# Kernel tuning notes

Measured on AMD Instinct MI355X. Metric: run time of the kernel, lower is better.

Reference implementation:

```python
import jax, jax.numpy as jnp
import numpy as np

SOFTMAX_SCALE = 10.0  # self.softmax_scale
EPS = 1e-4


def _patches(img, k=3):
    # img: [H, W, C] -> patches laid out as conv filters [k, k, C, L], L = H*W
    # (matches tf.image.extract_patches SAME/stride1 + reshape + transpose([0,2,3,4,1]))
    H, W, C = img.shape
    pad = (k - 1) // 2
    xp = jnp.pad(img, ((pad, pad), (pad, pad), (0, 0)))
    pat = jnp.stack([jnp.stack([xp[p:p + H, q:q + W] for q in range(k)]) for p in range(k)])
    # pat: [k, k, H, W, C] -> [k, k, C, H*W]; L index is row-major (h*W + w) like TF reshape
    return pat.transpose(0, 1, 4, 2, 3).reshape(k, k, C, H * W)


def _normed(p):
    # per-patch L2 normalization over the k*k*C axes (axes 0,1,2)
    return p / jnp.maximum(jnp.sqrt(jnp.sum(p * p, axis=(0, 1, 2))), EPS)


def _corr_recon(a, b, k=3):
    # a, b: [H', W', C] shifted feature maps
    Hp, Wp, C = a.shape
    L = Hp * Wp
    pa = _patches(a, k)  # [k,k,C,L]
    pb = _patches(b, k)
    y = (_normed(pa) * _normed(pb)).reshape(k * k * C, L)
    att = y.T @ y                                   # [L, L] patch-correlation scores
    att = jax.nn.softmax(att.reshape(1, Hp, Wp, L) * SOFTMAX_SCALE, axis=3)
    dn = ('NHWC', 'HWIO', 'NHWC')
    # tf.nn.conv2d_transpose(att, filters=[k,k,C,L], stride=1, SAME); rate=1 so /rate**2 is a no-op
    ya = jax.lax.conv_transpose(att, pa, (1, 1), 'SAME', dimension_numbers=dn, transpose_kernel=True)[0]
    yb = jax.lax.conv_transpose(att, pb, (1, 1), 'SAME', dimension_numbers=dn, transpose_kernel=True)[0]
    return ya, yb  # each [H', W', C]


def _ecattn_single(xi):
    # xi: [H, W, C]
    left, right = xi[:-1], xi[1:]          # vertical neighbor pair, [H-1, W, C]
    top, bottom = xi[:, 1:], xi[:, :-1]    # horizontal neighbor pair, [H, W-1, C]
    yl, yr = _corr_recon(left, right)
    ylr = jnp.concatenate([yr[:1], (yr[1:] + yl[:-1]) * 0.5, yl[-1:]], axis=0)   # [H, W, C]
    yt, yb = _corr_recon(top, bottom)
    ytb = jnp.concatenate([yt[:, :1], (yt[:, 1:] + yb[:, :-1]) * 0.5, yb[:, -1:]], axis=1)  # [H, W, C]
    return (ylr + ytb) * 0.5


def setup_inputs() -> dict:
    key = jax.random.key(0)
    k1, k2 = jax.random.split(key)
    B, H, W, C = 4, 32, 32, 256
    x = jax.random.normal(k1, (B, H, W, C), dtype=jnp.float32)
    mask = jax.random.uniform(k2, (B, H, W, 1), dtype=jnp.float32)
    return {'x': x, 'mask': mask}


def reference(x, mask):
    # mask is accepted by the layer's call() but unused inside contextualAttention
    return jax.vmap(_ecattn_single)(x)
```

## Files before the change

### kernel.cpp

```cpp
#include <hip/hip_runtime.h>


typedef _Float16 half8 __attribute__((ext_vector_type(8)));
typedef _Float16 half8u __attribute__((ext_vector_type(8), aligned(4)));
typedef _Float16 half4h __attribute__((ext_vector_type(4)));
typedef _Float16 half4u __attribute__((ext_vector_type(4), aligned(8)));
typedef float floatx4 __attribute__((ext_vector_type(4)));

constexpr int NL = 992, NC = 256, NC2 = 512;
constexpr int NLL = NL * NL;
constexpr int OFF_ABT = 0;
constexpr int OFF_MH  = OFF_ABT + NL * NC2 / 2;
constexpr int OFF_SA  = OFF_MH + NL * NC / 2;
constexpr int OFF_SB  = OFF_SA + 1024;
constexpr int OFF_INV = OFF_SA + 2048;
constexpr int OFF_Y   = OFF_SA + 3072;
constexpr int OFF_B0  = OFF_Y + NL * NC2;
constexpr int OFF_B1  = OFF_B0 + NLL / 2;
constexpr int TSTRIDE = OFF_B1 + NLL / 2;

__device__ __forceinline__ void gload16(const void* g, void* l) {
    __builtin_amdgcn_global_load_lds(
        (const __attribute__((address_space(1))) unsigned int*)g,
        (__attribute__((address_space(3))) unsigned int*)(unsigned long)(uintptr_t)l,
        16, 0, 0);
}

__global__ __launch_bounds__(256) void k_stage(const float* __restrict__ x,
                                               float* __restrict__ ws) {
    const int t = blockIdx.x & 7;
    const int l0 = (blockIdx.x >> 3) * 32;
    const int s = t >> 1, o = t & 1;
    float* wst = ws + (size_t)t * TSTRIDE;
    _Float16* __restrict__ ABt = (_Float16*)(wst + OFF_ABT);
    _Float16* __restrict__ Mh = (_Float16*)(wst + OFF_MH);
    __shared__ float Ta[32 * 33], Tb[32 * 33];
    const int tid = threadIdx.x;
    const int li = tid >> 3, cq = tid & 7;
    const int l = l0 + li;
    int aoff, boff;
    if (o == 0) {
        const int lh = l >> 5, lw = l & 31;
        aoff = ((s * 32 + lh) * 32 + lw) * NC;
        boff = aoff + 32 * NC;
    } else {
        const int lh = l / 31, lw = l - lh * 31;
        boff = ((s * 32 + lh) * 32 + lw) * NC;
        aoff = boff + NC;
    }
    float sa = 0.0f, sb = 0.0f;
    for (int cc = 0; cc < 8; ++cc) {
        const int c0 = cc * 32;
        const float4 a4 = *(const float4*)&x[aoff + c0 + cq * 4];
        const float4 b4 = *(const float4*)&x[boff + c0 + cq * 4];
        half4h m;
        m[0] = (_Float16)(a4.x * b4.x); m[1] = (_Float16)(a4.y * b4.y);
        m[2] = (_Float16)(a4.z * b4.z); m[3] = (_Float16)(a4.w * b4.w);
        *(half4u*)&Mh[l * NC + c0 + cq * 4] = m;
        sa += a4.x * a4.x + a4.y * a4.y + a4.z * a4.z + a4.w * a4.w;
        sb += b4.x * b4.x + b4.y * b4.y + b4.z * b4.z + b4.w * b4.w;
        __syncthreads();
        Ta[(cq * 4 + 0) * 33 + li] = a4.x; Tb[(cq * 4 + 0) * 33 + li] = b4.x;
        Ta[(cq * 4 + 1) * 33 + li] = a4.y; Tb[(cq * 4 + 1) * 33 + li] = b4.y;
        Ta[(cq * 4 + 2) * 33 + li] = a4.z; Tb[(cq * 4 + 2) * 33 + li] = b4.z;
        Ta[(cq * 4 + 3) * 33 + li] = a4.w; Tb[(cq * 4 + 3) * 33 + li] = b4.w;
        __syncthreads();
        const int ci = li, lq = cq;
        half4h ha, hb;
#pragma unroll
        for (int j = 0; j < 4; ++j) {
            ha[j] = (_Float16)Ta[ci * 33 + lq * 4 + j];
            hb[j] = (_Float16)Tb[ci * 33 + lq * 4 + j];
        }
        *(half4u*)&ABt[(c0 + ci) * NL + l0 + lq * 4] = ha;
        *(half4u*)&ABt[(NC + c0 + ci) * NL + l0 + lq * 4] = hb;
    }
#pragma unroll
    for (int off = 4; off > 0; off >>= 1) {
        sa += __shfl_down(sa, off, 8);
        sb += __shfl_down(sb, off, 8);
    }
    if (cq == 0) {
        wst[OFF_SA + l] = sa;
        wst[OFF_SB + l] = sb;
    }
}

__global__ __launch_bounds__(1024) void k_inv(float* __restrict__ ws) {
    const int t = blockIdx.x;
    const int l = threadIdx.x;
    if (l >= NL) return;
    const int o = t & 1;
    const int Hp = o ? 32 : 31, Wp = o ? 31 : 32;
    float* wst = ws + (size_t)t * TSTRIDE;
    const int h = l / Wp, w = l - h * Wp;
    float na2 = 0.0f, nb2 = 0.0f;
#pragma unroll
    for (int dh = -1; dh <= 1; ++dh)
#pragma unroll
        for (int dw = -1; dw <= 1; ++dw) {
            const int hh = h + dh, ww = w + dw;
            if ((unsigned)hh < (unsigned)Hp && (unsigned)ww < (unsigned)Wp) {
                const int ll = hh * Wp + ww;
                na2 += wst[OFF_SA + ll];
                nb2 += wst[OFF_SB + ll];
            }
        }
    const float na = fmaxf(sqrtf(na2), 1e-4f);
    const float nb = fmaxf(sqrtf(nb2), 1e-4f);
    wst[OFF_INV + l] = 1.0f / (na * nb);
}

__global__ __launch_bounds__(256) void k_gram(float* __restrict__ ws) {
    const int t = blockIdx.x & 7;
    const int u = blockIdx.x >> 3;
    const int i0 = (u >> 3) * 128, j0 = (u & 7) * 128;
    float* wst = ws + (size_t)t * TSTRIDE;
    const _Float16* __restrict__ M = (const _Float16*)(wst + OFF_MH);
    _Float16* __restrict__ S = (_Float16*)(wst + OFF_B0);
    __shared__ __align__(16) _Float16 As[128 * 32];
    __shared__ __align__(16) _Float16 Bs[128 * 32];
    const int tid = threadIdx.x;
    const int wave = tid >> 6, lane = tid & 63;
    const int wm = wave & 1, wn = wave >> 1;
    const int l15 = lane & 15, quad = lane >> 4;
    floatx4 acc[4][4] = {};
    const int srow = tid >> 2;
    const int scol = (tid & 3) * 8;
    for (int k0 = 0; k0 < NC; k0 += 32) {
        __syncthreads();
        if (i0 + srow < NL)      gload16(&M[(i0 + srow) * NC + k0 + scol], &As[srow * 32 + scol]);
        if (i0 + 64 + srow < NL) gload16(&M[(i0 + 64 + srow) * NC + k0 + scol], &As[(64 + srow) * 32 + scol]);
        if (j0 + srow < NL)      gload16(&M[(j0 + srow) * NC + k0 + scol], &Bs[srow * 32 + scol]);
        if (j0 + 64 + srow < NL) gload16(&M[(j0 + 64 + srow) * NC + k0 + scol], &Bs[(64 + srow) * 32 + scol]);
        __syncthreads();
        half8 a[4], b[4];
#pragma unroll
        for (int mt = 0; mt < 4; ++mt) a[mt] = *(const half8*)&As[(wm * 64 + mt * 16 + l15) * 32 + quad * 8];
#pragma unroll
        for (int nt = 0; nt < 4; ++nt) b[nt] = *(const half8*)&Bs[(wn * 64 + nt * 16 + l15) * 32 + quad * 8];
#pragma unroll
        for (int mt = 0; mt < 4; ++mt)
#pragma unroll
            for (int nt = 0; nt < 4; ++nt)
                acc[mt][nt] = __builtin_amdgcn_mfma_f32_16x16x32_f16(a[mt], b[nt], acc[mt][nt], 0, 0, 0);
    }
#pragma unroll
    for (int mt = 0; mt < 4; ++mt)
#pragma unroll
        for (int nt = 0; nt < 4; ++nt)
#pragma unroll
            for (int r = 0; r < 4; ++r) {
                const int row = i0 + wm * 64 + mt * 16 + quad * 4 + r;
                const int col = j0 + wn * 64 + nt * 16 + l15;
                if (row < NL && col < NL) S[row * NL + col] = (_Float16)acc[mt][nt][r];
            }
}

template<int WP, int HP>
__device__ __forceinline__ void softmax9_body(float* __restrict__ wst,
                                              const int l1, const int tid) {
    const _Float16* __restrict__ S = (const _Float16*)(wst + OFF_B0);
    const float* __restrict__ inv = wst + OFF_INV;
    _Float16* __restrict__ Ph = (_Float16*)(wst + OFF_B1);
    const int c0 = tid * 4;
    const int h1 = l1 / WP, w1 = l1 % WP;
    float lg[4] = {-3.0e38f, -3.0e38f, -3.0e38f, -3.0e38f};
    float mx = -3.0e38f;
    if (tid < 248) {
        int hc[4], wc[4];
#pragma unroll
        for (int j = 0; j < 4; ++j) { hc[j] = (c0 + j) / WP; wc[j] = (c0 + j) % WP; }
        float g[4] = {0.f, 0.f, 0.f, 0.f};
        const _Float16* base = S + l1 * NL + c0;
#pragma unroll
        for (int dh = -1; dh <= 1; ++dh) {
            const bool oh1 = (unsigned)(h1 + dh) < (unsigned)HP;
#pragma unroll
            for (int dw = -1; dw <= 1; ++dw) {
                const int sh = dh * WP + dw;
                const int par = sh & 1;
                const bool ok1 = oh1 && (unsigned)(w1 + dw) < (unsigned)WP;
                const half8u v = *(const half8u*)(base + sh * (NL + 1) - par);
#pragma unroll
                for (int j = 0; j < 4; ++j) {
                    const bool ok = ok1 && (unsigned)(hc[j] + dh) < (unsigned)HP &&
                                           (unsigned)(wc[j] + dw) < (unsigned)WP;
                    if (ok) g[j] += (float)v[j + par];
                }
            }
        }
        const float inv1 = inv[l1] * 10.0f;
#pragma unroll
        for (int j = 0; j < 4; ++j) {
            lg[j] = g[j] * inv1 * inv[c0 + j];
            mx = fmaxf(mx, lg[j]);
        }
    }
    __shared__ float red[4];
    const int wave = tid >> 6, lane = tid & 63;
#pragma unroll
    for (int off = 32; off > 0; off >>= 1) mx = fmaxf(mx, __shfl_down(mx, off));
    if (lane == 0) red[wave] = mx;
    __syncthreads();
    mx = fmaxf(fmaxf(red[0], red[1]), fmaxf(red[2], red[3]));
    __syncthreads();
    float e[4];
    float sum = 0.0f;
#pragma unroll
    for (int j = 0; j < 4; ++j) { e[j] = __expf(lg[j] - mx); sum += e[j]; }
    if (tid >= 248) sum = 0.0f;
#pragma unroll
    for (int off = 32; off > 0; off >>= 1) sum += __shfl_down(sum, off);
    if (lane == 0) red[wave] = sum;
    __syncthreads();
    sum = red[0] + red[1] + red[2] + red[3];
    const float rs = 1.0f / sum;
    if (tid < 248) {
        half4h o;
#pragma unroll
        for (int j = 0; j < 4; ++j) o[j] = (_Float16)(e[j] * rs);
        *(half4u*)(Ph + l1 * NL + c0) = o;
    }
}

__global__ __launch_bounds__(256) void k_softmax9(float* __restrict__ ws) {
    const int t = blockIdx.x & 7;
    const int l1 = blockIdx.x >> 3;
    float* wst = ws + (size_t)t * TSTRIDE;
    if (t & 1) softmax9_body<31, 32>(wst, l1, threadIdx.x);
    else       softmax9_body<32, 31>(wst, l1, threadIdx.x);
}

template<int WP, int HP>
__device__ __forceinline__ void band9p_body(float* __restrict__ wst,
                                            const int m, const int tid) {
    if (tid >= 248) return;
    const _Float16* __restrict__ P = (const _Float16*)(wst + OFF_B1);
    _Float16* __restrict__ W = (_Float16*)(wst + OFF_B0);
    const int c0 = tid * 4;
    const int hm = m / WP, wm = m % WP;
    int hc[4], wc[4];
#pragma unroll
    for (int j = 0; j < 4; ++j) { hc[j] = (c0 + j) / WP; wc[j] = (c0 + j) % WP; }
    float acc[4] = {0.f, 0.f, 0.f, 0.f};
    const _Float16* base = P + m * NL + c0;
#pragma unroll
    for (int dh = -1; dh <= 1; ++dh) {
        const bool oh1 = (unsigned)(hm + dh) < (unsigned)HP;
#pragma unroll
        for (int dw = -1; dw <= 1; ++dw) {
            const int sh = dh * WP + dw;
            const int par = sh & 1;
            const bool ok1 = oh1 && (unsigned)(wm + dw) < (unsigned)WP;
            const half8u v = *(const half8u*)(base + sh * (NL + 1) - par);
#pragma unroll
            for (int j = 0; j < 4; ++j) {
                const bool ok = ok1 && (unsigned)(hc[j] + dh) < (unsigned)HP &&
                                       (unsigned)(wc[j] + dw) < (unsigned)WP;
                if (ok) acc[j] += (float)v[j + par];
            }
        }
    }
    half4h o;
#pragma unroll
    for (int j = 0; j < 4; ++j) o[j] = (_Float16)acc[j];
    *(half4u*)(W + m * NL + c0) = o;
}

__global__ __launch_bounds__(256) void k_band9p(float* __restrict__ ws) {
    const int t = blockIdx.x & 7;
    const int m = blockIdx.x >> 3;
    float* wst = ws + (size_t)t * TSTRIDE;
    if (t & 1) band9p_body<31, 32>(wst, m, threadIdx.x);
    else       band9p_body<32, 31>(wst, m, threadIdx.x);
}

__global__ __launch_bounds__(256) void k_recon(float* __restrict__ ws) {
    const int t = blockIdx.x & 7;
    const int u = blockIdx.x >> 3;
    const int i0 = (u >> 2) * 128, j0 = (u & 3) * 128;
    float* wst = ws + (size_t)t * TSTRIDE;
    const _Float16* __restrict__ Wm = (const _Float16*)(wst + OFF_B0);
    const _Float16* __restrict__ ABt = (const _Float16*)(wst + OFF_ABT);
    float* __restrict__ Y = wst + OFF_Y;
    __shared__ __align__(16) _Float16 As[128 * 32];
    __shared__ __align__(16) _Float16 Bs[128 * 32];
    const int tid = threadIdx.x;
    const int wave = tid >> 6, lane = tid & 63;
    const int wm = wave & 1, wn = wave >> 1;
    const int l15 = lane & 15, quad = lane >> 4;
    floatx4 acc[4][4] = {};
    const int srow = tid >> 2;
    const int scol = (tid & 3) * 8;
    for (int k0 = 0; k0 < NL; k0 += 32) {
        __syncthreads();
        if (i0 + srow < NL)      gload16(&Wm[(i0 + srow) * NL + k0 + scol], &As[srow * 32 + scol]);
        if (i0 + 64 + srow < NL) gload16(&Wm[(i0 + 64 + srow) * NL + k0 + scol], &As[(64 + srow) * 32 + scol]);
        gload16(&ABt[(j0 + srow) * NL + k0 + scol], &Bs[srow * 32 + scol]);
        gload16(&ABt[(j0 + 64 + srow) * NL + k0 + scol], &Bs[(64 + srow) * 32 + scol]);
        __syncthreads();
        half8 a[4], b[4];
#pragma unroll
        for (int mt = 0; mt < 4; ++mt) a[mt] = *(const half8*)&As[(wm * 64 + mt * 16 + l15) * 32 + quad * 8];
#pragma unroll
        for (int nt = 0; nt < 4; ++nt) b[nt] = *(const half8*)&Bs[(wn * 64 + nt * 16 + l15) * 32 + quad * 8];
#pragma unroll
        for (int mt = 0; mt < 4; ++mt)
#pragma unroll
            for (int nt = 0; nt < 4; ++nt)
                acc[mt][nt] = __builtin_amdgcn_mfma_f32_16x16x32_f16(a[mt], b[nt], acc[mt][nt], 0, 0, 0);
    }
#pragma unroll
    for (int mt = 0; mt < 4; ++mt)
#pragma unroll
        for (int nt = 0; nt < 4; ++nt)
#pragma unroll
            for (int r = 0; r < 4; ++r) {
                const int row = i0 + wm * 64 + mt * 16 + quad * 4 + r;
                const int col = j0 + wn * 64 + nt * 16 + l15;
                if (row < NL) Y[row * NC2 + col] = acc[mt][nt][r];
            }
}

__global__ __launch_bounds__(256) void k_combine(float* __restrict__ out,
                                                 const float* __restrict__ ws) {
    const int idx = blockIdx.x;
    const int s = idx >> 10;
    const int hw = idx & 1023;
    const int h = hw >> 5, w = hw & 31;
    const int c = threadIdx.x;
    const float* Ylr = ws + (size_t)(2 * s) * TSTRIDE + OFF_Y;
    const float* Ytb = ws + (size_t)(2 * s + 1) * TSTRIDE + OFF_Y;
    float v = 0.0f;
    if (h < 31) v += Ylr[(h * 32 + w) * NC2 + NC + c] * (h == 0 ? 1.0f : 0.5f);
    if (h >= 1) v += Ylr[((h - 1) * 32 + w) * NC2 + c] * (h == 31 ? 1.0f : 0.5f);
    if (w < 31) v += Ytb[(h * 31 + w) * NC2 + c] * (w == 0 ? 1.0f : 0.5f);
    if (w >= 1) v += Ytb[(h * 31 + (w - 1)) * NC2 + NC + c] * (w == 31 ? 1.0f : 0.5f);
    out[(size_t)idx * NC + c] = v * 0.5f;
}

extern "C" void kernel_launch(void* const* d_in, const int* in_sizes, int n_in,
                              void* d_out, int out_size, void* d_ws, size_t ws_size,
                              hipStream_t stream) {
    const float* x = (const float*)d_in[0];
    float* out = (float*)d_out;
    float* ws = (float*)d_ws;

    hipLaunchKernelGGL(k_stage,    dim3(8 * 31), dim3(256),  0, stream, x, ws);
    hipLaunchKernelGGL(k_inv,      dim3(8),      dim3(1024), 0, stream, ws);
    hipLaunchKernelGGL(k_gram,     dim3(8 * 64), dim3(256),  0, stream, ws);
    hipLaunchKernelGGL(k_softmax9, dim3(8 * NL), dim3(256),  0, stream, ws);
    hipLaunchKernelGGL(k_band9p,   dim3(8 * NL), dim3(256),  0, stream, ws);
    hipLaunchKernelGGL(k_recon,    dim3(8 * 32), dim3(256),  0, stream, ws);
    hipLaunchKernelGGL(k_combine,  dim3(4096),   dim3(256),  0, stream, out, ws);
}
```

Measured before the change: 149.4 us.

## Shrink gram/recon tiles to 64x64, fold norm kernel into gram, store Y in fp16

The Gram and reconstruction GEMMs move from 128x128 to 64x64 output tiles, giving four times as many blocks so more CUs are busy; the Gram kernel also switches to a K step of 64. The separate inverse-norm kernel is removed and its work is done by block u==0 of the Gram kernel, saving one launch. The reconstruction output Y is stored as fp16 instead of fp32, halving its workspace and the traffic read by the combine kernel, at some precision cost. Smaller tiles lower data reuse per block.

```diff
diff --git a/kernel.cpp b/kernel.cpp
--- a/kernel.cpp
+++ b/kernel.cpp
@@ -15,7 +15,7 @@
 constexpr int OFF_SB  = OFF_SA + 1024;
 constexpr int OFF_INV = OFF_SA + 2048;
 constexpr int OFF_Y   = OFF_SA + 3072;
-constexpr int OFF_B0  = OFF_Y + NL * NC2;
+constexpr int OFF_B0  = OFF_Y + NL * NC2 / 2;
 constexpr int OFF_B1  = OFF_B0 + NLL / 2;
 constexpr int TSTRIDE = OFF_B1 + NLL / 2;
 
@@ -86,73 +86,80 @@
     }
 }
 
-__global__ __launch_bounds__(1024) void k_inv(float* __restrict__ ws) {
-    const int t = blockIdx.x;
-    const int l = threadIdx.x;
-    if (l >= NL) return;
-    const int o = t & 1;
-    const int Hp = o ? 32 : 31, Wp = o ? 31 : 32;
-    float* wst = ws + (size_t)t * TSTRIDE;
-    const int h = l / Wp, w = l - h * Wp;
-    float na2 = 0.0f, nb2 = 0.0f;
-#pragma unroll
-    for (int dh = -1; dh <= 1; ++dh)
-#pragma unroll
-        for (int dw = -1; dw <= 1; ++dw) {
-            const int hh = h + dh, ww = w + dw;
-            if ((unsigned)hh < (unsigned)Hp && (unsigned)ww < (unsigned)Wp) {
-                const int ll = hh * Wp + ww;
-                na2 += wst[OFF_SA + ll];
-                nb2 += wst[OFF_SB + ll];
-            }
-        }
-    const float na = fmaxf(sqrtf(na2), 1e-4f);
-    const float nb = fmaxf(sqrtf(nb2), 1e-4f);
-    wst[OFF_INV + l] = 1.0f / (na * nb);
-}
-
 __global__ __launch_bounds__(256) void k_gram(float* __restrict__ ws) {
     const int t = blockIdx.x & 7;
     const int u = blockIdx.x >> 3;
-    const int i0 = (u >> 3) * 128, j0 = (u & 7) * 128;
+    const int i0 = (u >> 4) * 64, j0 = (u & 15) * 64;
     float* wst = ws + (size_t)t * TSTRIDE;
     const _Float16* __restrict__ M = (const _Float16*)(wst + OFF_MH);
     _Float16* __restrict__ S = (_Float16*)(wst + OFF_B0);
-    __shared__ __align__(16) _Float16 As[128 * 32];
-    __shared__ __align__(16) _Float16 Bs[128 * 32];
     const int tid = threadIdx.x;
+
+    if (u == 0) {
+        const int o = t & 1;
+        const int Hp = o ? 32 : 31, Wp = o ? 31 : 32;
+#pragma unroll
+        for (int q = 0; q < 4; ++q) {
+            const int l = tid + q * 256;
+            if (l < NL) {
+                const int h = l / Wp, w = l - h * Wp;
+                float na2 = 0.0f, nb2 = 0.0f;
+#pragma unroll
+                for (int dh = -1; dh <= 1; ++dh)
+#pragma unroll
+                    for (int dw = -1; dw <= 1; ++dw) {
+                        const int hh = h + dh, ww = w + dw;
+                        if ((unsigned)hh < (unsigned)Hp && (unsigned)ww < (unsigned)Wp) {
+                            const int ll = hh * Wp + ww;
+                            na2 += wst[OFF_SA + ll];
+                            nb2 += wst[OFF_SB + ll];
+                        }
+                    }
+                const float na = fmaxf(sqrtf(na2), 1e-4f);
+                const float nb = fmaxf(sqrtf(nb2), 1e-4f);
+                wst[OFF_INV + l] = 1.0f / (na * nb);
+            }
+        }
+    }
+
+    __shared__ __align__(16) _Float16 As[64 * 64];
+    __shared__ __align__(16) _Float16 Bs[64 * 64];
     const int wave = tid >> 6, lane = tid & 63;
     const int wm = wave & 1, wn = wave >> 1;
     const int l15 = lane & 15, quad = lane >> 4;
-    floatx4 acc[4][4] = {};
-    const int srow = tid >> 2;
-    const int scol = (tid & 3) * 8;
-    for (int k0 = 0; k0 < NC; k0 += 32) {
-        __syncthreads();
-        if (i0 + srow < NL)      gload16(&M[(i0 + srow) * NC + k0 + scol], &As[srow * 32 + scol]);
-        if (i0 + 64 + srow < NL) gload16(&M[(i0 + 64 + srow) * NC + k0 + scol], &As[(64 + srow) * 32 + scol]);
-        if (j0 + srow < NL)      gload16(&M[(j0 + srow) * NC + k0 + scol], &Bs[srow * 32 + scol]);
-        if (j0 + 64 + srow < NL) gload16(&M[(j0 + 64 + srow) * NC + k0 + scol], &Bs[(64 + srow) * 32 + scol]);
-        __syncthreads();
-        half8 a[4], b[4];
-#pragma unroll
-        for (int mt = 0; mt < 4; ++mt) a[mt] = *(const half8*)&As[(wm * 64 + mt * 16 + l15) * 32 + quad * 8];
-#pragma unroll
-        for (int nt = 0; nt < 4; ++nt) b[nt] = *(const half8*)&Bs[(wn * 64 + nt * 16 + l15) * 32 + quad * 8];
-#pragma unroll
-        for (int mt = 0; mt < 4; ++mt)
-#pragma unroll
-            for (int nt = 0; nt < 4; ++nt)
-                acc[mt][nt] = __builtin_amdgcn_mfma_f32_16x16x32_f16(a[mt], b[nt], acc[mt][nt], 0, 0, 0);
-    }
-#pragma unroll
-    for (int mt = 0; mt < 4; ++mt)
-#pragma unroll
-        for (int nt = 0; nt < 4; ++nt)
+    floatx4 acc[2][2] = {};
+    for (int k0 = 0; k0 < NC; k0 += 64) {
+        __syncthreads();
+#pragma unroll
+        for (int rr = 0; rr < 2; ++rr) {
+            const int slot = tid + rr * 256;
+            const int row = slot >> 3, cg = (slot & 7) * 8;
+            if (i0 + row < NL) gload16(&M[(i0 + row) * NC + k0 + cg], &As[row * 64 + cg]);
+            if (j0 + row < NL) gload16(&M[(j0 + row) * NC + k0 + cg], &Bs[row * 64 + cg]);
+        }
+        __syncthreads();
+#pragma unroll
+        for (int kk = 0; kk < 2; ++kk) {
+            half8 a[2], b[2];
+#pragma unroll
+            for (int mt = 0; mt < 2; ++mt) a[mt] = *(const half8*)&As[(wm * 32 + mt * 16 + l15) * 64 + kk * 32 + quad * 8];
+#pragma unroll
+            for (int nt = 0; nt < 2; ++nt) b[nt] = *(const half8*)&Bs[(wn * 32 + nt * 16 + l15) * 64 + kk * 32 + quad * 8];
+#pragma unroll
+            for (int mt = 0; mt < 2; ++mt)
+#pragma unroll
+                for (int nt = 0; nt < 2; ++nt)
+                    acc[mt][nt] = __builtin_amdgcn_mfma_f32_16x16x32_f16(a[mt], b[nt], acc[mt][nt], 0, 0, 0);
+        }
+    }
+#pragma unroll
+    for (int mt = 0; mt < 2; ++mt)
+#pragma unroll
+        for (int nt = 0; nt < 2; ++nt)
 #pragma unroll
             for (int r = 0; r < 4; ++r) {
-                const int row = i0 + wm * 64 + mt * 16 + quad * 4 + r;
-                const int col = j0 + wn * 64 + nt * 16 + l15;
+                const int row = i0 + wm * 32 + mt * 16 + quad * 4 + r;
+                const int col = j0 + wn * 32 + nt * 16 + l15;
                 if (row < NL && col < NL) S[row * NL + col] = (_Float16)acc[mt][nt][r];
             }
 }
@@ -279,47 +286,44 @@
 __global__ __launch_bounds__(256) void k_recon(float* __restrict__ ws) {
     const int t = blockIdx.x & 7;
     const int u = blockIdx.x >> 3;
-    const int i0 = (u >> 2) * 128, j0 = (u & 3) * 128;
+    const int i0 = (u >> 3) * 64, j0 = (u & 7) * 64;
     float* wst = ws + (size_t)t * TSTRIDE;
     const _Float16* __restrict__ Wm = (const _Float16*)(wst + OFF_B0);
     const _Float16* __restrict__ ABt = (const _Float16*)(wst + OFF_ABT);
-    float* __restrict__ Y = wst + OFF_Y;
-    __shared__ __align__(16) _Float16 As[128 * 32];
-    __shared__ __align__(16) _Float16 Bs[128 * 32];
+    _Float16* __restrict__ Y = (_Float16*)(wst + OFF_Y);
+    __shared__ __align__(16) _Float16 As[64 * 32];
+    __shared__ __align__(16) _Float16 Bs[64 * 32];
     const int tid = threadIdx.x;
     const int wave = tid >> 6, lane = tid & 63;
     const int wm = wave & 1, wn = wave >> 1;
     const int l15 = lane & 15, quad = lane >> 4;
-    floatx4 acc[4][4] = {};
-    const int srow = tid >> 2;
-    const int scol = (tid & 3) * 8;
+    floatx4 acc[2][2] = {};
+    const int row = tid >> 2, cg = (tid & 3) * 8;
     for (int k0 = 0; k0 < NL; k0 += 32) {
         __syncthreads();
-        if (i0 + srow < NL)      gload16(&Wm[(i0 + srow) * NL + k0 + scol], &As[srow * 32 + scol]);
-        if (i0 + 64 + srow < NL) gload16(&Wm[(i0 + 64 + srow) * NL + k0 + scol], &As[(64 + srow) * 32 + scol]);
-        gload16(&ABt[(j0 + srow) * NL + k0 + scol], &Bs[srow * 32 + scol]);
-        gload16(&ABt[(j0 + 64 + srow) * NL + k0 + scol], &Bs[(64 + srow) * 32 + scol]);
-        __syncthreads();
-        half8 a[4], b[4];
-#pragma unroll
-        for (int mt = 0; mt < 4; ++mt) a[mt] = *(const half8*)&As[(wm * 64 + mt * 16 + l15) * 32 + quad * 8];
-#pragma unroll
-        for (int nt = 0; nt < 4; ++nt) b[nt] = *(const half8*)&Bs[(wn * 64 + nt * 16 + l15) * 32 + quad * 8];
-#pragma unroll
-        for (int mt = 0; mt < 4; ++mt)
-#pragma unroll
-            for (int nt = 0; nt < 4; ++nt)
+        if (i0 + row < NL) gload16(&Wm[(i0 + row) * NL + k0 + cg], &As[row * 32 + cg]);
+        gload16(&ABt[(j0 + row) * NL + k0 + cg], &Bs[row * 32 + cg]);
+        __syncthreads();
+        half8 a[2], b[2];
+#pragma unroll
+        for (int mt = 0; mt < 2; ++mt) a[mt] = *(const half8*)&As[(wm * 32 + mt * 16 + l15) * 32 + quad * 8];
+#pragma unroll
+        for (int nt = 0; nt < 2; ++nt) b[nt] = *(const half8*)&Bs[(wn * 32 + nt * 16 + l15) * 32 + quad * 8];
+#pragma unroll
+        for (int mt = 0; mt < 2; ++mt)
+#pragma unroll
+            for (int nt = 0; nt < 2; ++nt)
                 acc[mt][nt] = __builtin_amdgcn_mfma_f32_16x16x32_f16(a[mt], b[nt], acc[mt][nt], 0, 0, 0);
     }
 #pragma unroll
-    for (int mt = 0; mt < 4; ++mt)
-#pragma unroll
-        for (int nt = 0; nt < 4; ++nt)
+    for (int mt = 0; mt < 2; ++mt)
+#pragma unroll
+        for (int nt = 0; nt < 2; ++nt)
 #pragma unroll
             for (int r = 0; r < 4; ++r) {
-                const int row = i0 + wm * 64 + mt * 16 + quad * 4 + r;
-                const int col = j0 + wn * 64 + nt * 16 + l15;
-                if (row < NL) Y[row * NC2 + col] = acc[mt][nt][r];
+                const int rw = i0 + wm * 32 + mt * 16 + quad * 4 + r;
+                const int col = j0 + wn * 32 + nt * 16 + l15;
+                if (rw < NL) Y[rw * NC2 + col] = (_Float16)acc[mt][nt][r];
             }
 }
 
@@ -330,13 +334,13 @@
     const int hw = idx & 1023;
     const int h = hw >> 5, w = hw & 31;
     const int c = threadIdx.x;
-    const float* Ylr = ws + (size_t)(2 * s) * TSTRIDE + OFF_Y;
-    const float* Ytb = ws + (size_t)(2 * s + 1) * TSTRIDE + OFF_Y;
+    const _Float16* Ylr = (const _Float16*)(ws + (size_t)(2 * s) * TSTRIDE + OFF_Y);
+    const _Float16* Ytb = (const _Float16*)(ws + (size_t)(2 * s + 1) * TSTRIDE + OFF_Y);
     float v = 0.0f;
-    if (h < 31) v += Ylr[(h * 32 + w) * NC2 + NC + c] * (h == 0 ? 1.0f : 0.5f);
-    if (h >= 1) v += Ylr[((h - 1) * 32 + w) * NC2 + c] * (h == 31 ? 1.0f : 0.5f);
-    if (w < 31) v += Ytb[(h * 31 + w) * NC2 + c] * (w == 0 ? 1.0f : 0.5f);
-    if (w >= 1) v += Ytb[(h * 31 + (w - 1)) * NC2 + NC + c] * (w == 31 ? 1.0f : 0.5f);
+    if (h < 31) v += (float)Ylr[(h * 32 + w) * NC2 + NC + c] * (h == 0 ? 1.0f : 0.5f);
+    if (h >= 1) v += (float)Ylr[((h - 1) * 32 + w) * NC2 + c] * (h == 31 ? 1.0f : 0.5f);
+    if (w < 31) v += (float)Ytb[(h * 31 + w) * NC2 + c] * (w == 0 ? 1.0f : 0.5f);
+    if (w >= 1) v += (float)Ytb[(h * 31 + (w - 1)) * NC2 + NC + c] * (w == 31 ? 1.0f : 0.5f);
     out[(size_t)idx * NC + c] = v * 0.5f;
 }
 
@@ -347,11 +351,10 @@
     float* out = (float*)d_out;
     float* ws = (float*)d_ws;
 
-    hipLaunchKernelGGL(k_stage,    dim3(8 * 31), dim3(256),  0, stream, x, ws);
-    hipLaunchKernelGGL(k_inv,      dim3(8),      dim3(1024), 0, stream, ws);
-    hipLaunchKernelGGL(k_gram,     dim3(8 * 64), dim3(256),  0, stream, ws);
-    hipLaunchKernelGGL(k_softmax9, dim3(8 * NL), dim3(256),  0, stream, ws);
-    hipLaunchKernelGGL(k_band9p,   dim3(8 * NL), dim3(256),  0, stream, ws);
-    hipLaunchKernelGGL(k_recon,    dim3(8 * 32), dim3(256),  0, stream, ws);
-    hipLaunchKernelGGL(k_combine,  dim3(4096),   dim3(256),  0, stream, out, ws);
-}
+    hipLaunchKernelGGL(k_stage,    dim3(8 * 31),  dim3(256), 0, stream, x, ws);
+    hipLaunchKernelGGL(k_gram,     dim3(8 * 256), dim3(256), 0, stream, ws);
+    hipLaunchKernelGGL(k_softmax9, dim3(8 * NL),  dim3(256), 0, stream, ws);
+    hipLaunchKernelGGL(k_band9p,   dim3(8 * NL),  dim3(256), 0, stream, ws);
+    hipLaunchKernelGGL(k_recon,    dim3(8 * 128), dim3(256), 0, stream, ws);
+    hipLaunchKernelGGL(k_combine,  dim3(4096),    dim3(256), 0, stream, out, ws);
+}
```

Result: faster. 146.1 us (-2.2%).
